# Kernel tuning notes

Measured on AMD Instinct MI355X. Metric: run time of the kernel, lower is better.

Reference implementation:

```python
import jax, jax.numpy as jnp
import numpy as np

D_MODEL = 1024
N_HEADS = 16
D_HEAD = D_MODEL // N_HEADS
GN_EPS = 1e-5


def setup_inputs() -> dict:
    key = jax.random.key(0)
    ks = jax.random.split(key, 5)
    B, T = 2, 2048
    s = 1.0 / np.sqrt(D_MODEL)
    x = jax.random.normal(ks[0], (B, T, D_MODEL), dtype=jnp.float32)
    W_q = jax.random.normal(ks[1], (D_MODEL, D_MODEL), dtype=jnp.float32) * s
    W_k = jax.random.normal(ks[2], (D_MODEL, D_MODEL), dtype=jnp.float32) * s
    W_v = jax.random.normal(ks[3], (D_MODEL, D_MODEL), dtype=jnp.float32) * s
    W_o = jax.random.normal(ks[4], (D_MODEL, D_MODEL), dtype=jnp.float32) * s
    gn_weight = jnp.ones((D_MODEL,), dtype=jnp.float32)
    gn_bias = jnp.zeros((D_MODEL,), dtype=jnp.float32)
    return {"x": x, "W_q": W_q, "W_k": W_k, "W_v": W_v, "W_o": W_o,
            "gn_weight": gn_weight, "gn_bias": gn_bias}


def reference(x, W_q, W_k, W_v, W_o, gn_weight, gn_bias):
    B, T, _ = x.shape
    H, Dh = N_HEADS, D_HEAD
    # Projections (nn.Linear: y = x @ W.T), split heads -> [B, T, H, Dh]
    q = (x @ W_q.T).reshape(B, T, H, Dh)
    k = (x @ W_k.T).reshape(B, T, H, Dh)
    v = (x @ W_v.T).reshape(B, T, H, Dh)

    # Per-head causal decay mask D_h[i, j] = gamma_h^(i-j) for i >= j else 0
    gammas = jnp.asarray([1.0 - 2.0 ** (-5.0 - i) for i in range(H)],
                         dtype=jnp.float32)  # [H]
    idx = jnp.arange(T, dtype=jnp.float32)
    diff = idx[:, None] - idx[None, :]  # [T, T]
    decay = jnp.where(diff >= 0,
                      gammas[:, None, None] ** jnp.maximum(diff, 0.0),
                      0.0)  # [H, T, T]

    scale = jnp.sqrt(jnp.asarray(Dh, dtype=x.dtype))
    qk = jnp.einsum('bthd,bshd->bhts', q, k)          # [B, H, T, T]
    attn = qk * decay[None] / scale
    y = jnp.einsum('bhts,bshd->bthd', attn, v)        # [B, T, H, Dh]

    # GroupNorm(n_heads groups) over channels-last-transposed layout:
    # torch applies it to [B, d_model, T]; each group = one head's Dh channels,
    # normalized over (Dh, T).
    yg = y.transpose(0, 2, 3, 1)                      # [B, H, Dh, T]
    mean = yg.mean(axis=(2, 3), keepdims=True)
    var = yg.var(axis=(2, 3), keepdims=True)
    yn = (yg - mean) / jnp.sqrt(var + GN_EPS)
    yn = yn * gn_weight.reshape(1, H, Dh, 1) + gn_bias.reshape(1, H, Dh, 1)
    y = yn.transpose(0, 3, 1, 2).reshape(B, T, H * Dh)  # [B, T, d_model]
    return y @ W_o.T
```

## Files before the change

### kernel.cpp

```cpp
#include <hip/hip_runtime.h>
#include <math.h>

#define TSEQ 2048
#define NB   2
#define DM   1024
#define NH   16
#define DH   64
#define GN_EPS 1e-5f

typedef short v8s __attribute__((ext_vector_type(8)));
typedef short v4s __attribute__((ext_vector_type(4)));
typedef float v4f __attribute__((ext_vector_type(4)));

__device__ __forceinline__ short f2bf(float f) {
    union { float f; unsigned u; } c; c.f = f;
    unsigned u = c.u;
    unsigned r = (u + 0x7fffu + ((u >> 16) & 1u)) >> 16;
    return (short)r;
}
__device__ __forceinline__ float bf2f(short s) {
    union { unsigned u; float f; } c; c.u = ((unsigned)(unsigned short)s) << 16;
    return c.f;
}

__device__ __forceinline__ unsigned cvtpk_bf16(float lo, float hi) {
    unsigned r;
    asm("v_cvt_pk_bf16_f32 %0, %1, %2" : "=v"(r) : "v"(lo), "v"(hi));
    return r;
}

__device__ __forceinline__ void gl_lds16(const void* g, void* l) {
    __builtin_amdgcn_global_load_lds(
        (const __attribute__((address_space(1))) void*)g,
        (__attribute__((address_space(3))) void*)l, 16, 0, 0);
}

__global__ __launch_bounds__(256) void cast_kernel(
    const float* __restrict__ x,
    const float* __restrict__ Wq, const float* __restrict__ Wk,
    const float* __restrict__ Wv, const float* __restrict__ Wo,
    short* __restrict__ xbf, short* __restrict__ wbf)
{
    const int NX = NB * TSEQ * DM;
    const int NW = DM * DM;
    const int total4 = (NX + 4 * NW) / 4;
    for (int i = blockIdx.x * 256 + threadIdx.x; i < total4;
         i += gridDim.x * 256) {
        int e = i * 4;
        const float* src; short* dst;
        if (e < NX) { src = x + e; dst = xbf + e; }
        else {
            int o = e - NX;
            int w = o >> 20;
            int r = o & (NW - 1);
            src = (w == 0 ? Wq : w == 1 ? Wk : w == 2 ? Wv : Wo) + r;
            dst = wbf + o;
        }
        v4f v = *(const v4f*)src;
        v4s s;
        #pragma unroll
        for (int j = 0; j < 4; ++j) s[j] = f2bf(v[j]);
        *(v4s*)dst = s;
    }
}

__global__ __launch_bounds__(256, 3) void gemm_qkv_mfma(
    const short* __restrict__ xbf, const short* __restrict__ wbf,
    short* __restrict__ Qb, short* __restrict__ Kb,
    short* __restrict__ Kt, short* __restrict__ Vt)
{
    const int z = blockIdx.z;
    const short* __restrict__ Bmat = wbf + (size_t)z * (DM * DM);
    const int n0 = blockIdx.x * 128, m0 = blockIdx.y * 128;
    const int t = threadIdx.x, l = t & 63, w = t >> 6;
    const int wr = (w >> 1) * 64, wc = (w & 1) * 64;
    const int lr = l & 15, g = l >> 4, lg4 = g * 4;

    __shared__ short As[128 * 64];
    __shared__ short Bs[128 * 64];

    v4f acc[4][4];
    #pragma unroll
    for (int i = 0; i < 4; ++i)
        #pragma unroll
        for (int j = 0; j < 4; ++j) acc[i][j] = (v4f){0.f, 0.f, 0.f, 0.f};

    const char* Agp = (const char*)(xbf  + (size_t)m0 * DM);
    const char* Bgp = (const char*)(Bmat + (size_t)n0 * DM);

    int soff[4], sdst[4];
    #pragma unroll
    for (int p = 0; p < 4; ++p) {
        int i = p * 256 + t;
        int row = i >> 3;
        int cp  = (i & 7) * 16;
        soff[p] = row * (DM * 2) + (cp ^ ((row & 7) << 4));
        sdst[p] = (p * 256 + (t & 192)) * 16;
    }
    const int swz = (lr & 7) << 4;

    for (int kt = 0; kt < DM / 64; ++kt) {
        const int kb = kt * 128;
        #pragma unroll
        for (int p = 0; p < 4; ++p) {
            gl_lds16(Agp + (size_t)soff[p] + kb, (char*)As + sdst[p]);
            gl_lds16(Bgp + (size_t)soff[p] + kb, (char*)Bs + sdst[p]);
        }
        asm volatile("s_waitcnt vmcnt(0)" ::: "memory");
        __syncthreads();

        v8s bfr[4][2];
        #pragma unroll
        for (int j = 0; j < 4; ++j) {
            int rowb = wc + j * 16 + lr;
            #pragma unroll
            for (int ks = 0; ks < 2; ++ks)
                bfr[j][ks] = *(const v8s*)((const char*)Bs + rowb * 128
                               + ((ks * 64 + g * 16) ^ swz));
        }
        #pragma unroll
        for (int i = 0; i < 4; ++i) {
            int rowa = wr + i * 16 + lr;
            v8s a0 = *(const v8s*)((const char*)As + rowa * 128 + ((g * 16) ^ swz));
            v8s a1 = *(const v8s*)((const char*)As + rowa * 128 + ((64 + g * 16) ^ swz));
            #pragma unroll
            for (int j = 0; j < 4; ++j) {
                acc[i][j] = __builtin_amdgcn_mfma_f32_16x16x32_bf16(
                    a0, bfr[j][0], acc[i][j], 0, 0, 0);
                acc[i][j] = __builtin_amdgcn_mfma_f32_16x16x32_bf16(
                    a1, bfr[j][1], acc[i][j], 0, 0, 0);
            }
        }
        __syncthreads();
    }

    if (z == 0) {
        float l2gj[4];
        #pragma unroll
        for (int j = 0; j < 4; ++j) {
            int hh = (n0 + wc + j * 16 + lr) >> 6;
            l2gj[j] = log2f(1.0f - exp2f(-5.0f - (float)hh));
        }
        #pragma unroll
        for (int i = 0; i < 4; ++i) {
            int row = m0 + wr + i * 16 + lg4;
            #pragma unroll
            for (int j = 0; j < 4; ++j) {
                int col = n0 + wc + j * 16 + lr;
                #pragma unroll
                for (int r = 0; r < 4; ++r) {
                    int tl = (row + r) & 63;
                    float fac = exp2f(fmaf(l2gj[j], (float)tl, -3.0f));
                    Qb[(size_t)(row + r) * DM + col] = f2bf(acc[i][j][r] * fac);
                }
            }
        }
    } else if (z == 1) {
        float l2gj[4];
        #pragma unroll
        for (int j = 0; j < 4; ++j) {
            int hh = (n0 + wc + j * 16 + lr) >> 6;
            l2gj[j] = -log2f(1.0f - exp2f(-5.0f - (float)hh));
        }
        #pragma unroll
        for (int i = 0; i < 4; ++i) {
            int row  = m0 + wr + i * 16 + lg4;
            int bidx = row >> 11, tb = row & (TSEQ - 1);
            #pragma unroll
            for (int j = 0; j < 4; ++j) {
                int col = n0 + wc + j * 16 + lr;
                v4s pk;
                #pragma unroll
                for (int r = 0; r < 4; ++r) {
                    int tl = (row + r) & 63;
                    float fac = exp2f(l2gj[j] * (float)tl);
                    short bv = f2bf(acc[i][j][r] * fac);
                    Kb[(size_t)(row + r) * DM + col] = bv;
                    pk[r] = bv;
                }
                *(v4s*)(Kt + ((size_t)bidx << 21) + ((size_t)col << 11) + tb) = pk;
            }
        }
    } else {
        #pragma unroll
        for (int i = 0; i < 4; ++i) {
            int row  = m0 + wr + i * 16 + lg4;
            int bidx = row >> 11, tb = row & (TSEQ - 1);
            #pragma unroll
            for (int j = 0; j < 4; ++j) {
                int col = n0 + wc + j * 16 + lr;
                v4s pk;
                #pragma unroll
                for (int r = 0; r < 4; ++r) pk[r] = f2bf(acc[i][j][r]);
                *(v4s*)(Vt + ((size_t)bidx << 21) + ((size_t)col << 11) + tb) = pk;
            }
        }
    }
}

__global__ __launch_bounds__(256, 2) void chunk_kv(
    const short* __restrict__ Kt, const short* __restrict__ Vt,
    short* __restrict__ At)
{
    const int bid = blockIdx.x;
    const int c = bid & 31, bh = bid >> 5;
    const int b = bh >> 4, h = bh & 15;
    const int tid = threadIdx.x, l = tid & 63, w = tid >> 6;
    const int lr = l & 15, g = l >> 4;

    const size_t rowbase = ((size_t)b * DM + h * 64);

    v8s kf[2], vf[4][2];
    {
        const short* kp = Kt + (rowbase + 16 * w + lr) * TSEQ + 64 * c;
        kf[0] = *(const v8s*)(kp + g * 8);
        kf[1] = *(const v8s*)(kp + 32 + g * 8);
    }
    #pragma unroll
    for (int j = 0; j < 4; ++j) {
        const short* vp = Vt + (rowbase + j * 16 + lr) * TSEQ + 64 * c;
        vf[j][0] = *(const v8s*)(vp + g * 8);
        vf[j][1] = *(const v8s*)(vp + 32 + g * 8);
    }

    v4f acc[4];
    #pragma unroll
    for (int j = 0; j < 4; ++j) acc[j] = (v4f){0.f, 0.f, 0.f, 0.f};

    #pragma unroll
    for (int j = 0; j < 4; ++j) {
        acc[j] = __builtin_amdgcn_mfma_f32_16x16x32_bf16(kf[0], vf[j][0], acc[j], 0, 0, 0);
        acc[j] = __builtin_amdgcn_mfma_f32_16x16x32_bf16(kf[1], vf[j][1], acc[j], 0, 0, 0);
    }

    short* Ab = At + (((size_t)bh * 32 + c) << 12);
    #pragma unroll
    for (int j = 0; j < 4; ++j) {
        v4s pk;
        #pragma unroll
        for (int r = 0; r < 4; ++r) pk[r] = f2bf(acc[j][r]);
        *(v4s*)(Ab + (j * 16 + lr) * 64 + 16 * w + g * 4) = pk;
    }
}

__global__ __launch_bounds__(256) void chunk_scan(
    const short* __restrict__ At, short* __restrict__ St)
{
    const int idx = blockIdx.x * 256 + threadIdx.x;
    const int bh = idx >> 12;
    const int h  = bh & 15;
    const float l2g = log2f(1.0f - exp2f(-5.0f - (float)h));
    const float g64 = exp2f(l2g * 64.0f);

    const size_t base = ((size_t)bh << 17) + (idx & 4095);
    float state = 0.0f;
    #pragma unroll
    for (int c = 1; c < 32; ++c) {
        float a = bf2f(At[base + ((size_t)(c - 1) << 12)]);
        state = g64 * (state + a);
        St[base + ((size_t)c << 12)] = f2bf(state);
    }
}

__global__ __launch_bounds__(256, 2) void chunk_out(
    const short* __restrict__ Qb, const short* __restrict__ Kb,
    const short* __restrict__ Vt, const short* __restrict__ St,
    float* __restrict__ Y, float* __restrict__ psums)
{
    const int bid = blockIdx.x;
    const int xcd = bid & 7, r8 = bid >> 3;
    const int bh  = xcd * 4 + (r8 >> 5);
    const int c   = r8 & 31;
    const int b = bh >> 4, h = bh & 15;
    const int tid = threadIdx.x, l = tid & 63, w = tid >> 6;
    const int lr = l & 15, g = l >> 4;

    __shared__ short strip[64 * 64];
    __shared__ float tr[64][68];
    __shared__ float red[8];

    const size_t rowQK = ((size_t)(b * TSEQ + 64 * c)) * DM + h * 64;

    v8s qf[4][2];
    #pragma unroll
    for (int j = 0; j < 4; ++j) {
        const short* qp = Qb + rowQK + (size_t)(j * 16 + lr) * DM;
        qf[j][0] = *(const v8s*)(qp + g * 8);
        qf[j][1] = *(const v8s*)(qp + 32 + g * 8);
    }
    v8s kf0, kf1;
    {
        const short* kp = Kb + rowQK + (size_t)(16 * w + lr) * DM;
        kf0 = *(const v8s*)(kp + g * 8);
        kf1 = *(const v8s*)(kp + 32 + g * 8);
    }
    v8s sf0 = {}, sf1 = {};
    if (c > 0) {
        const short* sp = St + (((size_t)bh * 32 + c) << 12) + (16 * w + lr) * 64;
        sf0 = *(const v8s*)(sp + g * 8);
        sf1 = *(const v8s*)(sp + 32 + g * 8);
    }
    v8s vf0, vf1;
    {
        const short* vp = Vt + ((size_t)(b * DM + h * 64) + 16 * w + lr) * TSEQ
                          + 64 * c;
        vf0 = *(const v8s*)(vp + g * 8);
        vf1 = *(const v8s*)(vp + 32 + g * 8);
    }

    v4f s[4];
    #pragma unroll
    for (int j = 0; j < 4; ++j) {
        v4f a = (v4f){0.f, 0.f, 0.f, 0.f};
        a = __builtin_amdgcn_mfma_f32_16x16x32_bf16(kf0, qf[j][0], a, 0, 0, 0);
        a = __builtin_amdgcn_mfma_f32_16x16x32_bf16(kf1, qf[j][1], a, 0, 0, 0);
        s[j] = a;
    }

    v4f y[4];
    #pragma unroll
    for (int j = 0; j < 4; ++j) y[j] = (v4f){0.f, 0.f, 0.f, 0.f};
    if (c > 0) {
        #pragma unroll
        for (int j = 0; j < 4; ++j) {
            y[j] = __builtin_amdgcn_mfma_f32_16x16x32_bf16(sf0, qf[j][0], y[j], 0, 0, 0);
            y[j] = __builtin_amdgcn_mfma_f32_16x16x32_bf16(sf1, qf[j][1], y[j], 0, 0, 0);
        }
    }

    #pragma unroll
    for (int j = 0; j < 4; ++j) {
        v4f vv = s[j];
        #pragma unroll
        for (int r = 0; r < 4; ++r)
            if ((j * 16 + lr) - (16 * w + g * 4 + r) < 0) vv[r] = 0.0f;
        unsigned u0 = cvtpk_bf16(vv[0], vv[1]);
        unsigned u1 = cvtpk_bf16(vv[2], vv[3]);
        int byte = ((j * 16 + lr) * 128 + 32 * w + g * 8) ^ ((lr & 7) << 4);
        *(unsigned long long*)((char*)strip + byte) =
            (unsigned long long)u0 | ((unsigned long long)u1 << 32);
    }
    __syncthreads();

    #pragma unroll
    for (int j = 0; j < 4; ++j) {
        int rb = (j * 16 + lr) * 128;
        int sw = (lr & 7) << 4;
        v8s sB0 = *(const v8s*)((char*)strip + ((rb + g * 16) ^ sw));
        v8s sB1 = *(const v8s*)((char*)strip + ((rb + 64 + g * 16) ^ sw));
        y[j] = __builtin_amdgcn_mfma_f32_16x16x32_bf16(vf0, sB0, y[j], 0, 0, 0);
        y[j] = __builtin_amdgcn_mfma_f32_16x16x32_bf16(vf1, sB1, y[j], 0, 0, 0);
    }

    float lsum = 0.f, lsq = 0.f;
    #pragma unroll
    for (int j = 0; j < 4; ++j)
        #pragma unroll
        for (int r = 0; r < 4; ++r) {
            float vy = y[j][r];
            lsum += vy; lsq += vy * vy;
        }
    #pragma unroll
    for (int m = 32; m; m >>= 1) {
        lsum += __shfl_xor(lsum, m, 64);
        lsq  += __shfl_xor(lsq,  m, 64);
    }
    if (l == 0) { red[w] = lsum; red[4 + w] = lsq; }

    #pragma unroll
    for (int j = 0; j < 4; ++j)
        #pragma unroll
        for (int r = 0; r < 4; ++r)
            tr[j * 16 + lr][16 * w + g * 4 + r] = y[j][r];
    __syncthreads();

    if (tid == 0) {
        float* ps = psums + ((size_t)bh * 32 + c) * 2;
        ps[0] = red[0] + red[1] + red[2] + red[3];
        ps[1] = red[4] + red[5] + red[6] + red[7];
    }

    #pragma unroll
    for (int u = 0; u < 4; ++u) {
        int row  = (tid >> 4) + u * 16;
        int col4 = (tid & 15) * 4;
        *(v4f*)&Y[(size_t)(b * TSEQ + 64 * c + row) * DM + h * 64 + col4] =
            *(const v4f*)&tr[row][col4];
    }
}

__global__ __launch_bounds__(256) void gn_finalize(
    const float* __restrict__ psums,
    const float* __restrict__ gnw, const float* __restrict__ gnb,
    float* __restrict__ scale, float* __restrict__ shift)
{
    int idx = blockIdx.x * 256 + threadIdx.x;
    if (idx >= NB * DM) return;
    int bb = idx >> 10;
    int ch = idx & (DM - 1);
    int hh = ch >> 6;
    int bh = bb * 16 + hh;

    float s = 0.f, q = 0.f;
    #pragma unroll
    for (int k = 0; k < 32; ++k) {
        s += psums[((size_t)bh * 32 + k) * 2];
        q += psums[((size_t)bh * 32 + k) * 2 + 1];
    }
    const float n = (float)(DH * TSEQ);
    float mean = s / n;
    float var  = q / n - mean * mean;
    float rstd = rsqrtf(var + GN_EPS);
    float sc = rstd * gnw[ch];
    scale[idx] = sc;
    shift[idx] = gnb[ch] - mean * sc;
}

__global__ __launch_bounds__(256) void gn_apply(
    const float* __restrict__ Y, const float* __restrict__ scale,
    const float* __restrict__ shift, short* __restrict__ Ybf)
{
    const int total4 = (NB * TSEQ * DM) / 4;
    for (int i = blockIdx.x * 256 + threadIdx.x; i < total4;
         i += gridDim.x * 256) {
        int e = i * 4;
        int c = e & (DM - 1);
        int bb = e >> 21;
        v4f yv = *(const v4f*)(Y + e);
        v4f sc = *(const v4f*)(scale + bb * DM + c);
        v4f sh = *(const v4f*)(shift + bb * DM + c);
        v4s o;
        #pragma unroll
        for (int j = 0; j < 4; ++j) o[j] = f2bf(yv[j] * sc[j] + sh[j]);
        *(v4s*)(Ybf + e) = o;
    }
}

__global__ __launch_bounds__(256, 3) void gemm_out_mfma(
    const short* __restrict__ Ybf, const short* __restrict__ Wob,
    float* __restrict__ out)
{
    const int n0 = blockIdx.x * 128, m0 = blockIdx.y * 128;
    const int t = threadIdx.x, l = t & 63, w = t >> 6;
    const int wr = (w >> 1) * 64, wc = (w & 1) * 64;
    const int lr = l & 15, g = l >> 4;

    __shared__ short As[128 * 64];
    __shared__ short Bs[128 * 64];

    v4f acc[4][4];
    #pragma unroll
    for (int i = 0; i < 4; ++i)
        #pragma unroll
        for (int j = 0; j < 4; ++j) acc[i][j] = (v4f){0.f, 0.f, 0.f, 0.f};

    const char* Agp = (const char*)(Ybf + (size_t)m0 * DM);
    const char* Bgp = (const char*)(Wob + (size_t)n0 * DM);

    int soff[4], sdst[4];
    #pragma unroll
    for (int p = 0; p < 4; ++p) {
        int i = p * 256 + t;
        int row = i >> 3;
        int cp  = (i & 7) * 16;
        soff[p] = row * (DM * 2) + (cp ^ ((row & 7) << 4));
        sdst[p] = (p * 256 + (t & 192)) * 16;
    }
    const int swz = (lr & 7) << 4;

    for (int kt = 0; kt < DM / 64; ++kt) {
        const int kb = kt * 128;
        #pragma unroll
        for (int p = 0; p < 4; ++p) {
            gl_lds16(Agp + (size_t)soff[p] + kb, (char*)As + sdst[p]);
            gl_lds16(Bgp + (size_t)soff[p] + kb, (char*)Bs + sdst[p]);
        }
        asm volatile("s_waitcnt vmcnt(0)" ::: "memory");
        __syncthreads();

        v8s bfr[4][2];
        #pragma unroll
        for (int j = 0; j < 4; ++j) {
            int rowb = wc + j * 16 + lr;
            #pragma unroll
            for (int ks = 0; ks < 2; ++ks)
                bfr[j][ks] = *(const v8s*)((const char*)Bs + rowb * 128
                               + ((ks * 64 + g * 16) ^ swz));
        }
        #pragma unroll
        for (int i = 0; i < 4; ++i) {
            int rowa = wr + i * 16 + lr;
            v8s a0 = *(const v8s*)((const char*)As + rowa * 128 + ((g * 16) ^ swz));
            v8s a1 = *(const v8s*)((const char*)As + rowa * 128 + ((64 + g * 16) ^ swz));
            #pragma unroll
            for (int j = 0; j < 4; ++j) {
                acc[i][j] = __builtin_amdgcn_mfma_f32_16x16x32_bf16(
                    a0, bfr[j][0], acc[i][j], 0, 0, 0);
                acc[i][j] = __builtin_amdgcn_mfma_f32_16x16x32_bf16(
                    a1, bfr[j][1], acc[i][j], 0, 0, 0);
            }
        }
        __syncthreads();
    }

    #pragma unroll
    for (int i = 0; i < 4; ++i) {
        int row = m0 + wr + i * 16 + g * 4;
        #pragma unroll
        for (int j = 0; j < 4; ++j) {
            int col = n0 + wc + j * 16 + lr;
            #pragma unroll
            for (int r = 0; r < 4; ++r)
                out[(size_t)(row + r) * DM + col] = acc[i][j][r];
        }
    }
}

extern "C" void kernel_launch(void* const* d_in, const int* in_sizes, int n_in,
                              void* d_out, int out_size, void* d_ws, size_t ws_size,
                              hipStream_t stream)
{
    const float* x   = (const float*)d_in[0];
    const float* Wq  = (const float*)d_in[1];
    const float* Wk  = (const float*)d_in[2];
    const float* Wv  = (const float*)d_in[3];
    const float* Wo  = (const float*)d_in[4];
    const float* gnw = (const float*)d_in[5];
    const float* gnb = (const float*)d_in[6];
    float* out = (float*)d_out;

    char* wsb = (char*)d_ws;
    size_t o = 0;
    float* Y    = (float*)(wsb + o); o += (size_t)NB * TSEQ * DM * 4;
    short* Qb   = (short*)(wsb + o); o += (size_t)NB * TSEQ * DM * 2;
    short* Kb   = (short*)(wsb + o); o += (size_t)NB * TSEQ * DM * 2;
    short* Kt   = (short*)(wsb + o); o += (size_t)NB * TSEQ * DM * 2;
    short* Vt   = (short*)(wsb + o); o += (size_t)NB * TSEQ * DM * 2;
    short* xbf  = (short*)(wsb + o); o += (size_t)NB * TSEQ * DM * 2;
    short* wbf  = (short*)(wsb + o); o += (size_t)4 * DM * DM * 2;
    short* Ybf  = (short*)(wsb + o); o += (size_t)NB * TSEQ * DM * 2;
    float* psums = (float*)(wsb + o); o += (size_t)32 * 32 * 2 * 4;
    float* scale = (float*)(wsb + o); o += (size_t)NB * DM * 4;
    float* shift = (float*)(wsb + o); o += (size_t)NB * DM * 4;
    if (ws_size < o) return;

    short* At = xbf;
    short* St = Ybf;

    cast_kernel<<<2048, 256, 0, stream>>>(x, Wq, Wk, Wv, Wo, xbf, wbf);
    gemm_qkv_mfma<<<dim3(DM / 128, (NB * TSEQ) / 128, 3), 256, 0, stream>>>(
        xbf, wbf, Qb, Kb, Kt, Vt);
    chunk_kv<<<dim3(1024), 256, 0, stream>>>(Kt, Vt, At);
    chunk_scan<<<dim3(512), 256, 0, stream>>>(At, St);
    chunk_out<<<dim3(1024), 256, 0, stream>>>(Qb, Kb, Vt, St, Y, psums);
    gn_finalize<<<dim3((NB * DM + 255) / 256), 256, 0, stream>>>(
        psums, gnw, gnb, scale, shift);
    gn_apply<<<2048, 256, 0, stream>>>(Y, scale, shift, Ybf);
    gemm_out_mfma<<<dim3(DM / 128, (NB * TSEQ) / 128), 256, 0, stream>>>(
        Ybf, wbf + 3 * (size_t)DM * DM, out);
}
```

Measured before the change: 98.58 us.

## Rewrite QKV GEMM as 256x256 tile, 8-wave, double-buffered phased pipeline

Replaces the 128x128 single-buffered QKV GEMM with a 256x256 tile kernel using 512 threads, 128KB of double-buffered LDS, and a four-phase schedule. Each phase issues the next k-tile's global-to-LDS loads while MFMAs run on the current one. The grid is a 1D launch of 192 blocks with an XCD-aware tile remap, treating the Q/K/V weights as one concatenated N=3072 matrix. The epilogue decay factors now come from precomputed powers instead of a per-element exp2. The larger tile raises data reuse and hides load latency, but it lowers occupancy, uses more registers, and leaves fewer blocks to cover the GPU.

```diff
diff --git a/kernel.cpp b/kernel.cpp
--- a/kernel.cpp
+++ b/kernel.cpp
@@ -29,10 +29,10 @@
     return r;
 }
 
-__device__ __forceinline__ void gl_lds16(const void* g, void* l) {
+__device__ __forceinline__ void gl_lds16(const void* g, void* p) {
     __builtin_amdgcn_global_load_lds(
         (const __attribute__((address_space(1))) void*)g,
-        (__attribute__((address_space(3))) void*)l, 16, 0, 0);
+        (__attribute__((address_space(3))) void*)p, 16, 0, 0);
 }
 
 __global__ __launch_bounds__(256) void cast_kernel(
@@ -64,138 +64,200 @@
     }
 }
 
-__global__ __launch_bounds__(256, 3) void gemm_qkv_mfma(
+__global__ __launch_bounds__(512, 2) void gemm_qkv_8ph(
     const short* __restrict__ xbf, const short* __restrict__ wbf,
     short* __restrict__ Qb, short* __restrict__ Kb,
     short* __restrict__ Kt, short* __restrict__ Vt)
 {
-    const int z = blockIdx.z;
-    const short* __restrict__ Bmat = wbf + (size_t)z * (DM * DM);
-    const int n0 = blockIdx.x * 128, m0 = blockIdx.y * 128;
-    const int t = threadIdx.x, l = t & 63, w = t >> 6;
-    const int wr = (w >> 1) * 64, wc = (w & 1) * 64;
-    const int lr = l & 15, g = l >> 4, lg4 = g * 4;
-
-    __shared__ short As[128 * 64];
-    __shared__ short Bs[128 * 64];
-
-    v4f acc[4][4];
-    #pragma unroll
-    for (int i = 0; i < 4; ++i)
+    __shared__ char ldsb[131072];
+
+    const int bid = blockIdx.x;
+    const int gidx = (bid & 7) * 24 + (bid >> 3);
+    const int mt = gidx / 12, nt = gidx % 12;
+    const int m0 = mt * 256, n0 = nt * 256;
+
+    const int tid = threadIdx.x, l = tid & 63, w = tid >> 6;
+    const int lr = l & 15, kgrp = l >> 4;
+    const int wm = w >> 2, wn = w & 3;
+    const int swzl = (lr & 7) << 4;
+
+    const char* Axg = (const char*)xbf;
+    const char* Bwg = (const char*)wbf;
+
+    size_t srcA1[2], srcB2[2];
+    int    dstA1[2], dstB2[2];
+    #pragma unroll
+    for (int q = 0; q < 2; ++q) {
+        int c = w * 64 + l + 512 * q;
+        int u = c & 7;
+        int rowA = ((c >> 9) << 7) + ((c >> 3) & 63);
+        srcA1[q] = (size_t)(m0 + rowA) * 2048 + (size_t)((u ^ (rowA & 7)) << 4);
+        int rowB = ((c >> 8) << 6) + ((c >> 3) & 31);
+        srcB2[q] = (size_t)(n0 + rowB) * 2048 + (size_t)((u ^ (rowB & 7)) << 4);
+        int rA0 = q * 128 + w * 8;
+        dstA1[q] = rA0 * 128;
+        int rB0 = 64 * ((w >> 2) + 2 * q) + (w & 3) * 8;
+        dstB2[q] = 32768 + rB0 * 128;
+    }
+
+#define ISSUE_G1(tt) { int bo = ((tt) & 1) * 65536; size_t kb = (size_t)(tt) * 128; \
+    gl_lds16(Axg + srcA1[0] + kb, ldsb + bo + dstA1[0]); \
+    gl_lds16(Axg + srcA1[1] + kb, ldsb + bo + dstA1[1]); }
+#define ISSUE_G2(tt) { int bo = ((tt) & 1) * 65536; size_t kb = (size_t)(tt) * 128; \
+    gl_lds16(Bwg + srcB2[0] + kb, ldsb + bo + dstB2[0]); \
+    gl_lds16(Bwg + srcB2[1] + kb, ldsb + bo + dstB2[1]); }
+#define ISSUE_G3(tt) { int bo = ((tt) & 1) * 65536; size_t kb = (size_t)(tt) * 128; \
+    gl_lds16(Bwg + srcB2[0] + 32 * 2048 + kb, ldsb + bo + dstB2[0] + 32 * 128); \
+    gl_lds16(Bwg + srcB2[1] + 32 * 2048 + kb, ldsb + bo + dstB2[1] + 32 * 128); }
+#define ISSUE_G4(tt) { int bo = ((tt) & 1) * 65536; size_t kb = (size_t)(tt) * 128; \
+    gl_lds16(Axg + srcA1[0] + 64 * 2048 + kb, ldsb + bo + dstA1[0] + 64 * 128); \
+    gl_lds16(Axg + srcA1[1] + 64 * 2048 + kb, ldsb + bo + dstA1[1] + 64 * 128); }
+
+    v4f acc[8][4];
+    #pragma unroll
+    for (int i = 0; i < 8; ++i)
         #pragma unroll
         for (int j = 0; j < 4; ++j) acc[i][j] = (v4f){0.f, 0.f, 0.f, 0.f};
 
-    const char* Agp = (const char*)(xbf  + (size_t)m0 * DM);
-    const char* Bgp = (const char*)(Bmat + (size_t)n0 * DM);
-
-    int soff[4], sdst[4];
-    #pragma unroll
-    for (int p = 0; p < 4; ++p) {
-        int i = p * 256 + t;
-        int row = i >> 3;
-        int cp  = (i & 7) * 16;
-        soff[p] = row * (DM * 2) + (cp ^ ((row & 7) << 4));
-        sdst[p] = (p * 256 + (t & 192)) * 16;
-    }
-    const int swz = (lr & 7) << 4;
-
-    for (int kt = 0; kt < DM / 64; ++kt) {
-        const int kb = kt * 128;
-        #pragma unroll
-        for (int p = 0; p < 4; ++p) {
-            gl_lds16(Agp + (size_t)soff[p] + kb, (char*)As + sdst[p]);
-            gl_lds16(Bgp + (size_t)soff[p] + kb, (char*)Bs + sdst[p]);
-        }
-        asm volatile("s_waitcnt vmcnt(0)" ::: "memory");
-        __syncthreads();
-
-        v8s bfr[4][2];
-        #pragma unroll
-        for (int j = 0; j < 4; ++j) {
-            int rowb = wc + j * 16 + lr;
+    ISSUE_G1(0); ISSUE_G2(0); ISSUE_G3(0); ISSUE_G4(0);
+
+    v8s af[4][2], bfr[4][2];
+
+#define LDA(frl, frbase) { \
+    const char* rp = Ab + (wm * 128 + ((frbase) + (frl)) * 16 + lr) * 128; \
+    af[frl][0] = *(const v8s*)(rp + ((kgrp * 16) ^ swzl)); \
+    af[frl][1] = *(const v8s*)(rp + ((64 + kgrp * 16) ^ swzl)); }
+#define LDB(fc) { \
+    const char* rp = Bb + (wn * 64 + (fc) * 16 + lr) * 128; \
+    bfr[fc][0] = *(const v8s*)(rp + ((kgrp * 16) ^ swzl)); \
+    bfr[fc][1] = *(const v8s*)(rp + ((64 + kgrp * 16) ^ swzl)); }
+#define MM(frl, frbase, fc) \
+    acc[(frbase) + (frl)][fc] = __builtin_amdgcn_mfma_f32_16x16x32_bf16( \
+        af[frl][0], bfr[fc][0], acc[(frbase) + (frl)][fc], 0, 0, 0); \
+    acc[(frbase) + (frl)][fc] = __builtin_amdgcn_mfma_f32_16x16x32_bf16( \
+        af[frl][1], bfr[fc][1], acc[(frbase) + (frl)][fc], 0, 0, 0);
+
+    #pragma unroll 2
+    for (int t = 0; t < 16; ++t) {
+        const char* Ab = ldsb + (t & 1) * 65536;
+        const char* Bb = Ab + 32768;
+
+        asm volatile("s_waitcnt vmcnt(4)" ::: "memory");
+        __builtin_amdgcn_s_barrier();
+        __builtin_amdgcn_sched_barrier(0);
+        if (t < 15) ISSUE_G1(t + 1);
+        #pragma unroll
+        for (int frl = 0; frl < 4; ++frl) LDA(frl, 0);
+        LDB(0); LDB(1);
+        __builtin_amdgcn_s_setprio(1);
+        #pragma unroll
+        for (int frl = 0; frl < 4; ++frl) { MM(frl, 0, 0); MM(frl, 0, 1); }
+        __builtin_amdgcn_s_setprio(0);
+
+        if (t < 15) { asm volatile("s_waitcnt vmcnt(4)" ::: "memory"); }
+        else        { asm volatile("s_waitcnt vmcnt(2)" ::: "memory"); }
+        __builtin_amdgcn_s_barrier();
+        __builtin_amdgcn_sched_barrier(0);
+        if (t < 15) ISSUE_G2(t + 1);
+        LDB(2); LDB(3);
+        __builtin_amdgcn_s_setprio(1);
+        #pragma unroll
+        for (int frl = 0; frl < 4; ++frl) { MM(frl, 0, 2); MM(frl, 0, 3); }
+        __builtin_amdgcn_s_setprio(0);
+
+        if (t < 15) { asm volatile("s_waitcnt vmcnt(4)" ::: "memory"); }
+        else        { asm volatile("s_waitcnt vmcnt(0)" ::: "memory"); }
+        __builtin_amdgcn_s_barrier();
+        __builtin_amdgcn_sched_barrier(0);
+        if (t < 15) ISSUE_G3(t + 1);
+        #pragma unroll
+        for (int frl = 0; frl < 4; ++frl) LDA(frl, 4);
+        __builtin_amdgcn_s_setprio(1);
+        #pragma unroll
+        for (int frl = 0; frl < 4; ++frl) { MM(frl, 4, 0); MM(frl, 4, 1); }
+        __builtin_amdgcn_s_setprio(0);
+
+        if (t < 15) ISSUE_G4(t + 1);
+        __builtin_amdgcn_s_setprio(1);
+        #pragma unroll
+        for (int frl = 0; frl < 4; ++frl) { MM(frl, 4, 2); MM(frl, 4, 3); }
+        __builtin_amdgcn_s_setprio(0);
+    }
+
+    const int zz = n0 >> 10;
+    const int ncol0 = n0 & 1023;
+    const int rg = kgrp * 4;
+    const int rowbase = m0 + wm * 128;
+
+    if (zz == 0) {
+        #pragma unroll
+        for (int fc = 0; fc < 4; ++fc) {
+            int coll = ncol0 + wn * 64 + fc * 16 + lr;
+            int hh = coll >> 6;
+            float l2 = log2f(1.0f - exp2f(-5.0f - (float)hh));
+            float s1 = exp2f(l2);
+            float s16 = exp2f(l2 * 16.0f);
+            float e0 = exp2f(fmaf(l2, (float)rg, -3.0f));
+            float p16[4] = {1.f, s16, s16 * s16, s16 * s16 * s16};
+            float pr[4]  = {1.f, s1, s1 * s1, s1 * s1 * s1};
             #pragma unroll
-            for (int ks = 0; ks < 2; ++ks)
-                bfr[j][ks] = *(const v8s*)((const char*)Bs + rowb * 128
-                               + ((ks * 64 + g * 16) ^ swz));
-        }
-        #pragma unroll
-        for (int i = 0; i < 4; ++i) {
-            int rowa = wr + i * 16 + lr;
-            v8s a0 = *(const v8s*)((const char*)As + rowa * 128 + ((g * 16) ^ swz));
-            v8s a1 = *(const v8s*)((const char*)As + rowa * 128 + ((64 + g * 16) ^ swz));
+            for (int fr = 0; fr < 8; ++fr) {
+                float fb = e0 * p16[fr & 3];
+                int row = rowbase + fr * 16 + rg;
+                #pragma unroll
+                for (int r = 0; r < 4; ++r)
+                    Qb[(size_t)(row + r) * DM + coll] =
+                        f2bf(acc[fr][fc][r] * (fb * pr[r]));
+            }
+        }
+    } else if (zz == 1) {
+        #pragma unroll
+        for (int fc = 0; fc < 4; ++fc) {
+            int coll = ncol0 + wn * 64 + fc * 16 + lr;
+            int hh = coll >> 6;
+            float l2 = -log2f(1.0f - exp2f(-5.0f - (float)hh));
+            float s1 = exp2f(l2);
+            float s16 = exp2f(l2 * 16.0f);
+            float e0 = exp2f(l2 * (float)rg);
+            float p16[4] = {1.f, s16, s16 * s16, s16 * s16 * s16};
+            float pr[4]  = {1.f, s1, s1 * s1, s1 * s1 * s1};
             #pragma unroll
-            for (int j = 0; j < 4; ++j) {
-                acc[i][j] = __builtin_amdgcn_mfma_f32_16x16x32_bf16(
-                    a0, bfr[j][0], acc[i][j], 0, 0, 0);
-                acc[i][j] = __builtin_amdgcn_mfma_f32_16x16x32_bf16(
-                    a1, bfr[j][1], acc[i][j], 0, 0, 0);
-            }
-        }
-        __syncthreads();
-    }
-
-    if (z == 0) {
-        float l2gj[4];
-        #pragma unroll
-        for (int j = 0; j < 4; ++j) {
-            int hh = (n0 + wc + j * 16 + lr) >> 6;
-            l2gj[j] = log2f(1.0f - exp2f(-5.0f - (float)hh));
-        }
-        #pragma unroll
-        for (int i = 0; i < 4; ++i) {
-            int row = m0 + wr + i * 16 + lg4;
-            #pragma unroll
-            for (int j = 0; j < 4; ++j) {
-                int col = n0 + wc + j * 16 + lr;
-                #pragma unroll
-                for (int r = 0; r < 4; ++r) {
-                    int tl = (row + r) & 63;
-                    float fac = exp2f(fmaf(l2gj[j], (float)tl, -3.0f));
-                    Qb[(size_t)(row + r) * DM + col] = f2bf(acc[i][j][r] * fac);
-                }
-            }
-        }
-    } else if (z == 1) {
-        float l2gj[4];
-        #pragma unroll
-        for (int j = 0; j < 4; ++j) {
-            int hh = (n0 + wc + j * 16 + lr) >> 6;
-            l2gj[j] = -log2f(1.0f - exp2f(-5.0f - (float)hh));
-        }
-        #pragma unroll
-        for (int i = 0; i < 4; ++i) {
-            int row  = m0 + wr + i * 16 + lg4;
-            int bidx = row >> 11, tb = row & (TSEQ - 1);
-            #pragma unroll
-            for (int j = 0; j < 4; ++j) {
-                int col = n0 + wc + j * 16 + lr;
+            for (int fr = 0; fr < 8; ++fr) {
+                float fb = e0 * p16[fr & 3];
+                int row = rowbase + fr * 16 + rg;
+                int bidx = row >> 11, tb = row & (TSEQ - 1);
                 v4s pk;
                 #pragma unroll
                 for (int r = 0; r < 4; ++r) {
-                    int tl = (row + r) & 63;
-                    float fac = exp2f(l2gj[j] * (float)tl);
-                    short bv = f2bf(acc[i][j][r] * fac);
-                    Kb[(size_t)(row + r) * DM + col] = bv;
+                    short bv = f2bf(acc[fr][fc][r] * (fb * pr[r]));
+                    Kb[(size_t)(row + r) * DM + coll] = bv;
                     pk[r] = bv;
                 }
-                *(v4s*)(Kt + ((size_t)bidx << 21) + ((size_t)col << 11) + tb) = pk;
+                *(v4s*)(Kt + ((size_t)bidx << 21) + ((size_t)coll << 11) + tb) = pk;
             }
         }
     } else {
         #pragma unroll
-        for (int i = 0; i < 4; ++i) {
-            int row  = m0 + wr + i * 16 + lg4;
-            int bidx = row >> 11, tb = row & (TSEQ - 1);
+        for (int fc = 0; fc < 4; ++fc) {
+            int coll = ncol0 + wn * 64 + fc * 16 + lr;
             #pragma unroll
-            for (int j = 0; j < 4; ++j) {
-                int col = n0 + wc + j * 16 + lr;
+            for (int fr = 0; fr < 8; ++fr) {
+                int row = rowbase + fr * 16 + rg;
+                int bidx = row >> 11, tb = row & (TSEQ - 1);
                 v4s pk;
                 #pragma unroll
-                for (int r = 0; r < 4; ++r) pk[r] = f2bf(acc[i][j][r]);
-                *(v4s*)(Vt + ((size_t)bidx << 21) + ((size_t)col << 11) + tb) = pk;
+                for (int r = 0; r < 4; ++r) pk[r] = f2bf(acc[fr][fc][r]);
+                *(v4s*)(Vt + ((size_t)bidx << 21) + ((size_t)coll << 11) + tb) = pk;
             }
         }
     }
+#undef ISSUE_G1
+#undef ISSUE_G2
+#undef ISSUE_G3
+#undef ISSUE_G4
+#undef LDA
+#undef LDB
+#undef MM
 }
 
 __global__ __launch_bounds__(256, 2) void chunk_kv(
@@ -548,8 +610,7 @@
     short* St = Ybf;
 
     cast_kernel<<<2048, 256, 0, stream>>>(x, Wq, Wk, Wv, Wo, xbf, wbf);
-    gemm_qkv_mfma<<<dim3(DM / 128, (NB * TSEQ) / 128, 3), 256, 0, stream>>>(
-        xbf, wbf, Qb, Kb, Kt, Vt);
+    gemm_qkv_8ph<<<dim3(192), 512, 0, stream>>>(xbf, wbf, Qb, Kb, Kt, Vt);
     chunk_kv<<<dim3(1024), 256, 0, stream>>>(Kt, Vt, At);
     chunk_scan<<<dim3(512), 256, 0, stream>>>(At, St);
     chunk_out<<<dim3(1024), 256, 0, stream>>>(Qb, Kb, Vt, St, Y, psums);
```

Result: slower. 104.3 us (+5.8%).

## Fold GroupNorm affine into per-batch scaled W_o and output bias

Applied to the files above, without the earlier changes.

Instead of writing fp32 attention output and running a separate GroupNorm apply pass, chunk_out now writes raw bf16 output directly. A small wo_prep kernel scales W_o columns by the per-batch GN scale and computes a per-batch bias from the shift, and the output GEMM adds that bias in its epilogue. This removes a full fp32 write/read round trip of the activations. In exchange it adds a per-batch weight copy and rounds the un-normalized activations to bf16 before normalization, which may change accuracy.

```diff
diff --git a/kernel.cpp b/kernel.cpp
--- a/kernel.cpp
+++ b/kernel.cpp
@@ -265,7 +265,7 @@
 __global__ __launch_bounds__(256, 2) void chunk_out(
     const short* __restrict__ Qb, const short* __restrict__ Kb,
     const short* __restrict__ Vt, const short* __restrict__ St,
-    float* __restrict__ Y, float* __restrict__ psums)
+    short* __restrict__ Ybf, float* __restrict__ psums)
 {
     const int bid = blockIdx.x;
     const int xcd = bid & 7, r8 = bid >> 3;
@@ -384,8 +384,11 @@
     for (int u = 0; u < 4; ++u) {
         int row  = (tid >> 4) + u * 16;
         int col4 = (tid & 15) * 4;
-        *(v4f*)&Y[(size_t)(b * TSEQ + 64 * c + row) * DM + h * 64 + col4] =
-            *(const v4f*)&tr[row][col4];
+        v4f val = *(const v4f*)&tr[row][col4];
+        v4s pk;
+        #pragma unroll
+        for (int r = 0; r < 4; ++r) pk[r] = f2bf(val[r]);
+        *(v4s*)&Ybf[(size_t)(b * TSEQ + 64 * c + row) * DM + h * 64 + col4] = pk;
     }
 }
 
@@ -416,31 +419,51 @@
     shift[idx] = gnb[ch] - mean * sc;
 }
 
-__global__ __launch_bounds__(256) void gn_apply(
-    const float* __restrict__ Y, const float* __restrict__ scale,
-    const float* __restrict__ shift, short* __restrict__ Ybf)
-{
-    const int total4 = (NB * TSEQ * DM) / 4;
-    for (int i = blockIdx.x * 256 + threadIdx.x; i < total4;
-         i += gridDim.x * 256) {
-        int e = i * 4;
-        int c = e & (DM - 1);
-        int bb = e >> 21;
-        v4f yv = *(const v4f*)(Y + e);
-        v4f sc = *(const v4f*)(scale + bb * DM + c);
-        v4f sh = *(const v4f*)(shift + bb * DM + c);
-        v4s o;
-        #pragma unroll
-        for (int j = 0; j < 4; ++j) o[j] = f2bf(yv[j] * sc[j] + sh[j]);
-        *(v4s*)(Ybf + e) = o;
-    }
+__global__ __launch_bounds__(256) void wo_prep(
+    const short* __restrict__ Wob, const float* __restrict__ scale,
+    const float* __restrict__ shift,
+    short* __restrict__ Wo2, float* __restrict__ bias)
+{
+    const int tid = threadIdx.x, l = tid & 63, w = tid >> 6;
+    const int bn = blockIdx.x * 4 + w;
+    const int b = bn >> 10, n = bn & 1023;
+    const int k0 = l * 16;
+
+    const short* wp = Wob + (size_t)n * DM + k0;
+    v8s w0 = *(const v8s*)wp;
+    v8s w1 = *(const v8s*)(wp + 8);
+    const float* sc = scale + b * DM + k0;
+    const float* sh = shift + b * DM + k0;
+
+    v8s o0, o1;
+    float bsum = 0.f;
+    #pragma unroll
+    for (int j = 0; j < 8; ++j) {
+        float wf = bf2f(w0[j]);
+        o0[j] = f2bf(wf * sc[j]);
+        bsum = fmaf(sh[j], wf, bsum);
+    }
+    #pragma unroll
+    for (int j = 0; j < 8; ++j) {
+        float wf = bf2f(w1[j]);
+        o1[j] = f2bf(wf * sc[8 + j]);
+        bsum = fmaf(sh[8 + j], wf, bsum);
+    }
+    short* op = Wo2 + ((size_t)b * DM + n) * DM + k0;
+    *(v8s*)op = o0;
+    *(v8s*)(op + 8) = o1;
+
+    #pragma unroll
+    for (int m = 32; m; m >>= 1) bsum += __shfl_xor(bsum, m, 64);
+    if (l == 0) bias[bn] = bsum;
 }
 
 __global__ __launch_bounds__(256, 3) void gemm_out_mfma(
-    const short* __restrict__ Ybf, const short* __restrict__ Wob,
-    float* __restrict__ out)
+    const short* __restrict__ Ybf, const short* __restrict__ Wo2,
+    const float* __restrict__ bias, float* __restrict__ out)
 {
     const int n0 = blockIdx.x * 128, m0 = blockIdx.y * 128;
+    const int b = m0 >> 11;
     const int t = threadIdx.x, l = t & 63, w = t >> 6;
     const int wr = (w >> 1) * 64, wc = (w & 1) * 64;
     const int lr = l & 15, g = l >> 4;
@@ -455,7 +478,7 @@
         for (int j = 0; j < 4; ++j) acc[i][j] = (v4f){0.f, 0.f, 0.f, 0.f};
 
     const char* Agp = (const char*)(Ybf + (size_t)m0 * DM);
-    const char* Bgp = (const char*)(Wob + (size_t)n0 * DM);
+    const char* Bgp = (const char*)(Wo2 + (size_t)b * DM * DM + (size_t)n0 * DM);
 
     int soff[4], sdst[4];
     #pragma unroll
@@ -509,9 +532,10 @@
         #pragma unroll
         for (int j = 0; j < 4; ++j) {
             int col = n0 + wc + j * 16 + lr;
+            float bv = bias[b * DM + col];
             #pragma unroll
             for (int r = 0; r < 4; ++r)
-                out[(size_t)(row + r) * DM + col] = acc[i][j][r];
+                out[(size_t)(row + r) * DM + col] = acc[i][j][r] + bv;
         }
     }
 }
@@ -531,7 +555,6 @@
 
     char* wsb = (char*)d_ws;
     size_t o = 0;
-    float* Y    = (float*)(wsb + o); o += (size_t)NB * TSEQ * DM * 4;
     short* Qb   = (short*)(wsb + o); o += (size_t)NB * TSEQ * DM * 2;
     short* Kb   = (short*)(wsb + o); o += (size_t)NB * TSEQ * DM * 2;
     short* Kt   = (short*)(wsb + o); o += (size_t)NB * TSEQ * DM * 2;
@@ -539,23 +562,26 @@
     short* xbf  = (short*)(wsb + o); o += (size_t)NB * TSEQ * DM * 2;
     short* wbf  = (short*)(wsb + o); o += (size_t)4 * DM * DM * 2;
     short* Ybf  = (short*)(wsb + o); o += (size_t)NB * TSEQ * DM * 2;
+    short* St   = (short*)(wsb + o); o += (size_t)NB * TSEQ * DM * 2;
+    short* Wo2  = (short*)(wsb + o); o += (size_t)NB * DM * DM * 2;
     float* psums = (float*)(wsb + o); o += (size_t)32 * 32 * 2 * 4;
     float* scale = (float*)(wsb + o); o += (size_t)NB * DM * 4;
     float* shift = (float*)(wsb + o); o += (size_t)NB * DM * 4;
+    float* bias  = (float*)(wsb + o); o += (size_t)NB * DM * 4;
     if (ws_size < o) return;
 
     short* At = xbf;
-    short* St = Ybf;
 
     cast_kernel<<<2048, 256, 0, stream>>>(x, Wq, Wk, Wv, Wo, xbf, wbf);
     gemm_qkv_mfma<<<dim3(DM / 128, (NB * TSEQ) / 128, 3), 256, 0, stream>>>(
         xbf, wbf, Qb, Kb, Kt, Vt);
     chunk_kv<<<dim3(1024), 256, 0, stream>>>(Kt, Vt, At);
     chunk_scan<<<dim3(512), 256, 0, stream>>>(At, St);
-    chunk_out<<<dim3(1024), 256, 0, stream>>>(Qb, Kb, Vt, St, Y, psums);
+    chunk_out<<<dim3(1024), 256, 0, stream>>>(Qb, Kb, Vt, St, Ybf, psums);
     gn_finalize<<<dim3((NB * DM + 255) / 256), 256, 0, stream>>>(
         psums, gnw, gnb, scale, shift);
-    gn_apply<<<2048, 256, 0, stream>>>(Y, scale, shift, Ybf);
+    wo_prep<<<dim3(512), 256, 0, stream>>>(
+        wbf + 3 * (size_t)DM * DM, scale, shift, Wo2, bias);
     gemm_out_mfma<<<dim3(DM / 128, (NB * TSEQ) / 128), 256, 0, stream>>>(
-        Ybf, wbf + 3 * (size_t)DM * DM, out);
-}
+        Ybf, Wo2, bias, out);
+}
```

Result: faster. 95.69 us (-2.9%).
